# Optimization experiments

Hardware: AMD Instinct MI355X
Metric: run time of the kernel (lower is better)

Reference implementation:

```python
import jax, jax.numpy as jnp
import numpy as np

B, N, DIM, H, D = 4, 2048, 1024, 16, 64  # inner_dim = dim // n_heads
NEG_INF = float('-inf')


def setup_inputs() -> dict:
    key = jax.random.key(0)
    k1, k2, k3, k4 = jax.random.split(key, 4)
    x = jax.random.normal(k1, (B, N, DIM), dtype=jnp.float32)
    Wqkv = jax.random.normal(k2, (3 * H * D, DIM), dtype=jnp.float32) * (DIM ** -0.5)
    key_mask = jax.random.randint(k3, (B, N), 0, 2).astype(jnp.bool_)
    query_mask = jax.random.randint(k4, (B, N), 0, 2).astype(jnp.bool_)
    return {"x": x, "Wqkv": Wqkv, "key_mask": key_mask, "query_mask": query_mask, "causal": 1}


def reference(x, Wqkv, key_mask, query_mask, causal):
    # fused qkv projection (self-attention fast path)
    qkv = jnp.einsum('bnc,fc->bnf', x, Wqkv)  # [B, N, 3*H*D]
    q, k, v = jnp.split(qkv, 3, axis=-1)
    def to_heads(t):
        return t.reshape(B, N, H, D).transpose(0, 2, 1, 3)  # b h n d
    q, k, v = to_heads(q), to_heads(k), to_heads(v)

    attn = jnp.einsum('bhnd,bhmd->bhnm', q, k) / np.sqrt(D).astype(np.float32)

    # pairwise key/query mask: [B, 1, Nq, Nk]
    pair = key_mask[:, None, None, :] & query_mask[:, None, :, None]
    attn = attn + jnp.where(pair, 0.0, NEG_INF)

    if causal:
        causal_mask = jnp.triu(jnp.full((N, N), NEG_INF, dtype=attn.dtype), k=1)
        attn = attn + causal_mask

    attn = jax.nn.softmax(attn, axis=-1)
    attn = jnp.nan_to_num(attn, nan=0.0)  # fully-masked rows -> 0

    out = jnp.einsum('bhnm,bhmd->bhnd', attn, v)
    out = out.transpose(0, 2, 1, 3).reshape(B, N, H * D)  # b n (h d)
    # inner_dim * n_heads == dim, so out_proj is skipped (matches torch code)
    return out
```

## Files before the change

### kernel.cpp

```cpp
#include <hip/hip_runtime.h>
#include <hip/hip_bf16.h>

typedef unsigned short u16;
typedef __attribute__((ext_vector_type(8))) short bf16x8;
typedef __attribute__((ext_vector_type(4))) float f32x4;

#define Bdim 4
#define Nseq 2048
#define DIMc 1024
#define NH   16
#define HD   64
#define F3   3072
#define Mrows 8192

typedef const __attribute__((address_space(1))) unsigned int gl_u32;
typedef __attribute__((address_space(3))) unsigned int lds_u32;

static __device__ __forceinline__ u16 f2b(float f) {
    union { float f; unsigned u; } v; v.f = f;
    unsigned r = v.u + 0x7fffu + ((v.u >> 16) & 1u);
    return (u16)(r >> 16);
}

__global__ __launch_bounds__(256) void cast_f32_bf16_kernel(const float* __restrict__ in,
                                                            u16* __restrict__ out, int n4) {
    int i = blockIdx.x * 256 + threadIdx.x;
    if (i >= n4) return;
    float4 v = reinterpret_cast<const float4*>(in)[i];
    ushort4 o;
    o.x = f2b(v.x); o.y = f2b(v.y); o.z = f2b(v.z); o.w = f2b(v.w);
    reinterpret_cast<ushort4*>(out)[i] = o;
}

__global__ __launch_bounds__(256) void norm_mask_kernel(const void* __restrict__ raw, int n,
                                                        int* __restrict__ outm) {
    const unsigned* as_u = (const unsigned*)raw;
    const float* as_f = (const float*)raw;
    const unsigned char* as_b = (const unsigned char*)raw;
    int ns = n < 512 ? n : 512;
    bool ok_i = true, ok_f = true;
    for (int i = 0; i < ns; ++i) {
        unsigned v = as_u[i];
        ok_i &= (v <= 1u);
        ok_f &= (v == 0u) || (v == 0x3f800000u);
    }
    const int mode = ok_i ? 0 : (ok_f ? 1 : 2);
    int i = blockIdx.x * 256 + threadIdx.x;
    if (i < n) {
        int v;
        if (mode == 0) v = (int)as_u[i];
        else if (mode == 1) v = (as_f[i] != 0.f) ? 1 : 0;
        else v = (int)as_b[i];
        outm[i] = (v != 0) ? 1 : 0;
    }
}

__global__ __launch_bounds__(256, 2) void qkv_gemm_kernel(const u16* __restrict__ A,
                                                          const u16* __restrict__ Bw,
                                                          u16* __restrict__ C) {
    __shared__ u16 As[128 * 32];
    __shared__ u16 Bs[128 * 32];
    const int t = threadIdx.x;
    const int lane = t & 63;
    const int wave = t >> 6;
    const int wr = (wave >> 1) * 64;
    const int wc = (wave & 1) * 64;
    const int row0 = blockIdx.x * 128;
    const int col0 = blockIdx.y * 128;

    const int lr = lane & 15;
    const int lk = (lane >> 4) * 8;
    const int cr = (lane >> 4) * 4;
    const int cc = lane & 15;

    const f32x4 fzero = {0.f, 0.f, 0.f, 0.f};
    f32x4 acc[4][4];
#pragma unroll
    for (int i = 0; i < 4; ++i)
#pragma unroll
        for (int j = 0; j < 4; ++j) acc[i][j] = fzero;

    const int strow = wave * 16 + (lane >> 2);
    const int stcol = (lane & 3) * 8;

    for (int k0 = 0; k0 < DIMc; k0 += 32) {
        __syncthreads();
#pragma unroll
        for (int issue = 0; issue < 2; ++issue) {
            const int r = issue * 64 + strow;
            __builtin_amdgcn_global_load_lds(
                (gl_u32*)(A + (size_t)(row0 + r) * DIMc + k0 + stcol),
                (lds_u32*)(As + (size_t)(issue * 64 + wave * 16) * 32), 16, 0, 0);
            __builtin_amdgcn_global_load_lds(
                (gl_u32*)(Bw + (size_t)(col0 + r) * DIMc + k0 + stcol),
                (lds_u32*)(Bs + (size_t)(issue * 64 + wave * 16) * 32), 16, 0, 0);
        }
        __syncthreads();

        bf16x8 af[4], bfr[4];
#pragma unroll
        for (int i = 0; i < 4; ++i) {
            af[i]  = *reinterpret_cast<const bf16x8*>(&As[(wr + i * 16 + lr) * 32 + lk]);
            bfr[i] = *reinterpret_cast<const bf16x8*>(&Bs[(wc + i * 16 + lr) * 32 + lk]);
        }
#pragma unroll
        for (int mi = 0; mi < 4; ++mi)
#pragma unroll
            for (int ni = 0; ni < 4; ++ni)
                acc[mi][ni] = __builtin_amdgcn_mfma_f32_16x16x32_bf16(af[mi], bfr[ni], acc[mi][ni], 0, 0, 0);
    }

#pragma unroll
    for (int mi = 0; mi < 4; ++mi)
#pragma unroll
        for (int ni = 0; ni < 4; ++ni)
#pragma unroll
            for (int j = 0; j < 4; ++j) {
                int r = row0 + wr + mi * 16 + cr + j;
                int c = col0 + wc + ni * 16 + cc;
                C[(size_t)r * F3 + c] = f2b(acc[mi][ni][j]);
            }
}

static __device__ __forceinline__ void attn_tile_compute(
    const bf16x8 (&qfr)[2][2], const int (&qmv)[2],
    float (&mrow)[2], float (&lsum)[2], f32x4 (&oacc)[4][2],
    const bf16x8 (&ka)[4][2], const bf16x8 (&va)[4][2],
    const int (&km)[4][4],
    int wq0, int m0, int causal,
    u16 (*Psw)[72], int g, int lq)
{
    const f32x4 fzero = {0.f, 0.f, 0.f, 0.f};
    f32x4 sacc[4][2];
#pragma unroll
    for (int kf = 0; kf < 4; ++kf)
#pragma unroll
        for (int qf = 0; qf < 2; ++qf) sacc[kf][qf] = fzero;
#pragma unroll
    for (int kf = 0; kf < 4; ++kf)
#pragma unroll
        for (int qf = 0; qf < 2; ++qf) {
            sacc[kf][qf] = __builtin_amdgcn_mfma_f32_16x16x32_bf16(ka[kf][0], qfr[qf][0], sacc[kf][qf], 0, 0, 0);
            sacc[kf][qf] = __builtin_amdgcn_mfma_f32_16x16x32_bf16(ka[kf][1], qfr[qf][1], sacc[kf][qf], 0, 0, 0);
        }

#pragma unroll
    for (int qf = 0; qf < 2; ++qf) {
        const int qg = wq0 + qf * 16 + lq;
        const bool qok = (qmv[qf] != 0);
        float s[4][4];
        float mx = -1e30f;
#pragma unroll
        for (int kf = 0; kf < 4; ++kf)
#pragma unroll
            for (int r = 0; r < 4; ++r) {
                const int kg = m0 + kf * 16 + g * 4 + r;
                float sv = sacc[kf][qf][r] * 0.125f;
                const bool ok = qok && (km[kf][r] != 0) && (!causal || kg <= qg);
                sv = ok ? sv : -1e30f;
                s[kf][r] = sv;
                mx = fmaxf(mx, sv);
            }
        mx = fmaxf(mx, __shfl_xor(mx, 16));
        mx = fmaxf(mx, __shfl_xor(mx, 32));
        const float mnew = fmaxf(mrow[qf], mx);
        const float scale = __expf(mrow[qf] - mnew);
        float rs = 0.f;
#pragma unroll
        for (int kf = 0; kf < 4; ++kf)
#pragma unroll
            for (int r = 0; r < 4; ++r) {
                const float pv = (s[kf][r] > -1e29f) ? __expf(s[kf][r] - mnew) : 0.f;
                s[kf][r] = pv;
                rs += pv;
            }
        rs += __shfl_xor(rs, 16);
        rs += __shfl_xor(rs, 32);
        lsum[qf] = lsum[qf] * scale + rs;
        mrow[qf] = mnew;
#pragma unroll
        for (int df = 0; df < 4; ++df) oacc[df][qf] *= scale;
#pragma unroll
        for (int kf = 0; kf < 4; ++kf)
#pragma unroll
            for (int r = 0; r < 4; ++r)
                Psw[qf * 16 + lq][kf * 16 + g * 4 + r] = f2b(s[kf][r]);
    }

    bf16x8 pb[2][2];
#pragma unroll
    for (int qf = 0; qf < 2; ++qf)
#pragma unroll
        for (int kc = 0; kc < 2; ++kc)
            pb[qf][kc] = *reinterpret_cast<const bf16x8*>(&Psw[qf * 16 + lq][kc * 32 + g * 8]);
#pragma unroll
    for (int df = 0; df < 4; ++df)
#pragma unroll
        for (int qf = 0; qf < 2; ++qf) {
            oacc[df][qf] = __builtin_amdgcn_mfma_f32_16x16x32_bf16(va[df][0], pb[qf][0], oacc[df][qf], 0, 0, 0);
            oacc[df][qf] = __builtin_amdgcn_mfma_f32_16x16x32_bf16(va[df][1], pb[qf][1], oacc[df][qf], 0, 0, 0);
        }
}

__global__ __launch_bounds__(256, 2) void attn_kernel(const u16* __restrict__ qkv,
                                                      const int* __restrict__ key_mask,
                                                      const int* __restrict__ query_mask,
                                                      const int* __restrict__ causal_p,
                                                      float* __restrict__ out) {
    const int bh = blockIdx.x;
    const int p = blockIdx.y;
    const int b = bh >> 4;
    const int h = bh & 15;
    const int t = threadIdx.x;
    const int lane = t & 63;
    const int wave = t >> 6;
    const int g = lane >> 4;
    const int lq = lane & 15;
    const int causal = causal_p[0];

    __shared__ u16 Ks[64][72];
    __shared__ u16 Vt[64][72];
    __shared__ u16 Ps[4][32][72];

    const int q0A = p * 128;
    const int q0B = (15 - p) * 128;
    const int wq0A = q0A + wave * 32;
    const int wq0B = q0B + wave * 32;

    const f32x4 fzero = {0.f, 0.f, 0.f, 0.f};

    bf16x8 qfrA[2][2], qfrB[2][2];
#pragma unroll
    for (int qf = 0; qf < 2; ++qf)
#pragma unroll
        for (int ks = 0; ks < 2; ++ks) {
            qfrA[qf][ks] = *reinterpret_cast<const bf16x8*>(
                qkv + (size_t)(b * Nseq + wq0A + qf * 16 + lq) * F3 + h * HD + ks * 32 + g * 8);
            qfrB[qf][ks] = *reinterpret_cast<const bf16x8*>(
                qkv + (size_t)(b * Nseq + wq0B + qf * 16 + lq) * F3 + h * HD + ks * 32 + g * 8);
        }

    int qmA[2], qmB[2];
    float mrowA[2], lsumA[2], mrowB[2], lsumB[2];
    f32x4 oaccA[4][2], oaccB[4][2];
#pragma unroll
    for (int qf = 0; qf < 2; ++qf) {
        qmA[qf] = query_mask[b * Nseq + wq0A + qf * 16 + lq];
        qmB[qf] = query_mask[b * Nseq + wq0B + qf * 16 + lq];
        mrowA[qf] = -1e30f; lsumA[qf] = 0.f;
        mrowB[qf] = -1e30f; lsumB[qf] = 0.f;
    }
#pragma unroll
    for (int df = 0; df < 4; ++df)
#pragma unroll
        for (int qf = 0; qf < 2; ++qf) { oaccA[df][qf] = fzero; oaccB[df][qf] = fzero; }

    const int kvendA = causal ? (q0A + 128) : Nseq;
    const int kvendB = causal ? (q0B + 128) : Nseq;

    const int sr = t >> 2;
    const int sc = (t & 3) * 8;

    bf16x8 kr0, kr1, vr0, vr1;
    {
        const u16* krow = qkv + (size_t)(b * Nseq + 0 + sr) * F3 + DIMc + h * HD;
        kr0 = *reinterpret_cast<const bf16x8*>(krow + sc);
        kr1 = *reinterpret_cast<const bf16x8*>(krow + sc + 32);
        const u16* vrow = qkv + (size_t)(b * Nseq + 0 + lane) * F3 + 2 * DIMc + h * HD + wave * 16;
        vr0 = *reinterpret_cast<const bf16x8*>(vrow);
        vr1 = *reinterpret_cast<const bf16x8*>(vrow + 8);
    }

    for (int m0 = 0; m0 < kvendB; m0 += 64) {
        *reinterpret_cast<bf16x8*>(&Ks[sr][sc])      = kr0;
        *reinterpret_cast<bf16x8*>(&Ks[sr][sc + 32]) = kr1;
#pragma unroll
        for (int e = 0; e < 8; ++e) {
            Vt[wave * 16 + e][lane]     = (u16)vr0[e];
            Vt[wave * 16 + 8 + e][lane] = (u16)vr1[e];
        }
        __syncthreads();

        if (m0 + 64 < kvendB) {
            const u16* krow = qkv + (size_t)(b * Nseq + m0 + 64 + sr) * F3 + DIMc + h * HD;
            kr0 = *reinterpret_cast<const bf16x8*>(krow + sc);
            kr1 = *reinterpret_cast<const bf16x8*>(krow + sc + 32);
            const u16* vrow = qkv + (size_t)(b * Nseq + m0 + 64 + lane) * F3 + 2 * DIMc + h * HD + wave * 16;
            vr0 = *reinterpret_cast<const bf16x8*>(vrow);
            vr1 = *reinterpret_cast<const bf16x8*>(vrow + 8);
        }

        int km[4][4];
#pragma unroll
        for (int kf = 0; kf < 4; ++kf) {
            int4 k4 = *reinterpret_cast<const int4*>(key_mask + b * Nseq + m0 + kf * 16 + g * 4);
            km[kf][0] = k4.x; km[kf][1] = k4.y; km[kf][2] = k4.z; km[kf][3] = k4.w;
        }
        bf16x8 ka[4][2], va[4][2];
#pragma unroll
        for (int kf = 0; kf < 4; ++kf)
#pragma unroll
            for (int ks = 0; ks < 2; ++ks)
                ka[kf][ks] = *reinterpret_cast<const bf16x8*>(&Ks[kf * 16 + lq][ks * 32 + g * 8]);
#pragma unroll
        for (int df = 0; df < 4; ++df)
#pragma unroll
            for (int kc = 0; kc < 2; ++kc)
                va[df][kc] = *reinterpret_cast<const bf16x8*>(&Vt[df * 16 + lq][kc * 32 + g * 8]);

        attn_tile_compute(qfrB, qmB, mrowB, lsumB, oaccB, ka, va, km, wq0B, m0, causal,
                          Ps[wave], g, lq);
        if (m0 < kvendA)
            attn_tile_compute(qfrA, qmA, mrowA, lsumA, oaccA, ka, va, km, wq0A, m0, causal,
                              Ps[wave], g, lq);
        __syncthreads();
    }

#pragma unroll
    for (int qf = 0; qf < 2; ++qf) {
        const float invA = (mrowA[qf] > -1e29f && lsumA[qf] > 0.f) ? 1.f / lsumA[qf] : 0.f;
        const float invB = (mrowB[qf] > -1e29f && lsumB[qf] > 0.f) ? 1.f / lsumB[qf] : 0.f;
        const size_t rowA = (size_t)(b * Nseq + wq0A + qf * 16 + lq) * DIMc + h * HD;
        const size_t rowB = (size_t)(b * Nseq + wq0B + qf * 16 + lq) * DIMc + h * HD;
#pragma unroll
        for (int df = 0; df < 4; ++df)
#pragma unroll
            for (int r = 0; r < 4; ++r) {
                out[rowA + df * 16 + g * 4 + r] = oaccA[df][qf][r] * invA;
                out[rowB + df * 16 + g * 4 + r] = oaccB[df][qf][r] * invB;
            }
    }
}

extern "C" void kernel_launch(void* const* d_in, const int* in_sizes, int n_in,
                              void* d_out, int out_size, void* d_ws, size_t ws_size,
                              hipStream_t stream) {
    const float* x = (const float*)d_in[0];
    const float* W = (const float*)d_in[1];

    char* ws = (char*)d_ws;
    int* km_n = (int*)(ws);
    int* qm_n = (int*)(ws + 32 * 1024);
    int* ca_n = (int*)(ws + 64 * 1024);
    u16* qkv  = (u16*)(ws + (size_t)1024 * 1024);
    u16* xb   = (u16*)(ws + (size_t)49 * 1024 * 1024);
    u16* wb   = (u16*)(ws + (size_t)65 * 1024 * 1024);

    const int nm = Bdim * Nseq;
    norm_mask_kernel<<<(nm + 255) / 256, 256, 0, stream>>>(d_in[2], nm, km_n);
    norm_mask_kernel<<<(nm + 255) / 256, 256, 0, stream>>>(d_in[3], nm, qm_n);
    norm_mask_kernel<<<1, 256, 0, stream>>>(d_in[4], 1, ca_n);

    const int nx4 = (Mrows * DIMc) / 4;
    const int nw4 = (F3 * DIMc) / 4;
    cast_f32_bf16_kernel<<<(nx4 + 255) / 256, 256, 0, stream>>>(x, xb, nx4);
    cast_f32_bf16_kernel<<<(nw4 + 255) / 256, 256, 0, stream>>>(W, wb, nw4);

    qkv_gemm_kernel<<<dim3(Mrows / 128, F3 / 128), 256, 0, stream>>>(xb, wb, qkv);

    attn_kernel<<<dim3(Bdim * NH, 8), 256, 0, stream>>>(qkv, km_n, qm_n, ca_n,
                                                        (float*)d_out);
}
```

Measured before the change: 244.0 us.

## Halve attention query tile per wave and double grid for occupancy

Each wave now handles 16 query rows instead of 32 per tile pair, so each block covers 64+64 query rows and the grid doubles to 16 blocks per head along y. Register and LDS use shrink, launch bounds are raised to allow 4 blocks per CU, and the LDS row padding changes from 72 to 68. The intent is more parallel blocks and higher occupancy to hide latency. The cost is that each K/V tile loaded into LDS is reused across fewer queries, which raises total K/V traffic and synchronisation per unit of work.

```diff
diff --git a/kernel.cpp b/kernel.cpp
--- a/kernel.cpp
+++ b/kernel.cpp
@@ -12,6 +12,8 @@
 #define HD   64
 #define F3   3072
 #define Mrows 8192
+
+#define KPAD 68
 
 typedef const __attribute__((address_space(1))) unsigned int gl_u32;
 typedef __attribute__((address_space(3))) unsigned int lds_u32;
@@ -123,86 +125,75 @@
 }
 
 static __device__ __forceinline__ void attn_tile_compute(
-    const bf16x8 (&qfr)[2][2], const int (&qmv)[2],
-    float (&mrow)[2], float (&lsum)[2], f32x4 (&oacc)[4][2],
+    const bf16x8 (&qfr)[2], int qmv,
+    float& mrow, float& lsum, f32x4 (&oacc)[4],
     const bf16x8 (&ka)[4][2], const bf16x8 (&va)[4][2],
     const int (&km)[4][4],
     int wq0, int m0, int causal,
-    u16 (*Psw)[72], int g, int lq)
+    u16 (*Psw)[KPAD], int g, int lq)
 {
     const f32x4 fzero = {0.f, 0.f, 0.f, 0.f};
-    f32x4 sacc[4][2];
+    f32x4 sacc[4];
+#pragma unroll
+    for (int kf = 0; kf < 4; ++kf) sacc[kf] = fzero;
+#pragma unroll
+    for (int kf = 0; kf < 4; ++kf) {
+        sacc[kf] = __builtin_amdgcn_mfma_f32_16x16x32_bf16(ka[kf][0], qfr[0], sacc[kf], 0, 0, 0);
+        sacc[kf] = __builtin_amdgcn_mfma_f32_16x16x32_bf16(ka[kf][1], qfr[1], sacc[kf], 0, 0, 0);
+    }
+
+    const int qg = wq0 + lq;
+    const bool qok = (qmv != 0);
+    float s[4][4];
+    float mx = -1e30f;
 #pragma unroll
     for (int kf = 0; kf < 4; ++kf)
 #pragma unroll
-        for (int qf = 0; qf < 2; ++qf) sacc[kf][qf] = fzero;
+        for (int r = 0; r < 4; ++r) {
+            const int kg = m0 + kf * 16 + g * 4 + r;
+            float sv = sacc[kf][r] * 0.125f;
+            const bool ok = qok && (km[kf][r] != 0) && (!causal || kg <= qg);
+            sv = ok ? sv : -1e30f;
+            s[kf][r] = sv;
+            mx = fmaxf(mx, sv);
+        }
+    mx = fmaxf(mx, __shfl_xor(mx, 16));
+    mx = fmaxf(mx, __shfl_xor(mx, 32));
+    const float mnew = fmaxf(mrow, mx);
+    const float scale = __expf(mrow - mnew);
+    float rs = 0.f;
 #pragma unroll
     for (int kf = 0; kf < 4; ++kf)
 #pragma unroll
-        for (int qf = 0; qf < 2; ++qf) {
-            sacc[kf][qf] = __builtin_amdgcn_mfma_f32_16x16x32_bf16(ka[kf][0], qfr[qf][0], sacc[kf][qf], 0, 0, 0);
-            sacc[kf][qf] = __builtin_amdgcn_mfma_f32_16x16x32_bf16(ka[kf][1], qfr[qf][1], sacc[kf][qf], 0, 0, 0);
-        }
-
-#pragma unroll
-    for (int qf = 0; qf < 2; ++qf) {
-        const int qg = wq0 + qf * 16 + lq;
-        const bool qok = (qmv[qf] != 0);
-        float s[4][4];
-        float mx = -1e30f;
-#pragma unroll
-        for (int kf = 0; kf < 4; ++kf)
-#pragma unroll
-            for (int r = 0; r < 4; ++r) {
-                const int kg = m0 + kf * 16 + g * 4 + r;
-                float sv = sacc[kf][qf][r] * 0.125f;
-                const bool ok = qok && (km[kf][r] != 0) && (!causal || kg <= qg);
-                sv = ok ? sv : -1e30f;
-                s[kf][r] = sv;
-                mx = fmaxf(mx, sv);
-            }
-        mx = fmaxf(mx, __shfl_xor(mx, 16));
-        mx = fmaxf(mx, __shfl_xor(mx, 32));
-        const float mnew = fmaxf(mrow[qf], mx);
-        const float scale = __expf(mrow[qf] - mnew);
-        float rs = 0.f;
-#pragma unroll
-        for (int kf = 0; kf < 4; ++kf)
-#pragma unroll
-            for (int r = 0; r < 4; ++r) {
-                const float pv = (s[kf][r] > -1e29f) ? __expf(s[kf][r] - mnew) : 0.f;
-                s[kf][r] = pv;
-                rs += pv;
-            }
-        rs += __shfl_xor(rs, 16);
-        rs += __shfl_xor(rs, 32);
-        lsum[qf] = lsum[qf] * scale + rs;
-        mrow[qf] = mnew;
-#pragma unroll
-        for (int df = 0; df < 4; ++df) oacc[df][qf] *= scale;
-#pragma unroll
-        for (int kf = 0; kf < 4; ++kf)
-#pragma unroll
-            for (int r = 0; r < 4; ++r)
-                Psw[qf * 16 + lq][kf * 16 + g * 4 + r] = f2b(s[kf][r]);
-    }
-
-    bf16x8 pb[2][2];
-#pragma unroll
-    for (int qf = 0; qf < 2; ++qf)
-#pragma unroll
-        for (int kc = 0; kc < 2; ++kc)
-            pb[qf][kc] = *reinterpret_cast<const bf16x8*>(&Psw[qf * 16 + lq][kc * 32 + g * 8]);
-#pragma unroll
-    for (int df = 0; df < 4; ++df)
-#pragma unroll
-        for (int qf = 0; qf < 2; ++qf) {
-            oacc[df][qf] = __builtin_amdgcn_mfma_f32_16x16x32_bf16(va[df][0], pb[qf][0], oacc[df][qf], 0, 0, 0);
-            oacc[df][qf] = __builtin_amdgcn_mfma_f32_16x16x32_bf16(va[df][1], pb[qf][1], oacc[df][qf], 0, 0, 0);
-        }
-}
-
-__global__ __launch_bounds__(256, 2) void attn_kernel(const u16* __restrict__ qkv,
+        for (int r = 0; r < 4; ++r) {
+            const float pv = (s[kf][r] > -1e29f) ? __expf(s[kf][r] - mnew) : 0.f;
+            s[kf][r] = pv;
+            rs += pv;
+        }
+    rs += __shfl_xor(rs, 16);
+    rs += __shfl_xor(rs, 32);
+    lsum = lsum * scale + rs;
+    mrow = mnew;
+#pragma unroll
+    for (int df = 0; df < 4; ++df) oacc[df] *= scale;
+#pragma unroll
+    for (int kf = 0; kf < 4; ++kf)
+#pragma unroll
+        for (int r = 0; r < 4; ++r)
+            Psw[lq][kf * 16 + g * 4 + r] = f2b(s[kf][r]);
+
+    bf16x8 pb[2];
+#pragma unroll
+    for (int kc = 0; kc < 2; ++kc)
+        pb[kc] = *reinterpret_cast<const bf16x8*>(&Psw[lq][kc * 32 + g * 8]);
+#pragma unroll
+    for (int df = 0; df < 4; ++df) {
+        oacc[df] = __builtin_amdgcn_mfma_f32_16x16x32_bf16(va[df][0], pb[0], oacc[df], 0, 0, 0);
+        oacc[df] = __builtin_amdgcn_mfma_f32_16x16x32_bf16(va[df][1], pb[1], oacc[df], 0, 0, 0);
+    }
+}
+
+__global__ __launch_bounds__(256, 4) void attn_kernel(const u16* __restrict__ qkv,
                                                       const int* __restrict__ key_mask,
                                                       const int* __restrict__ query_mask,
                                                       const int* __restrict__ causal_p,
@@ -218,55 +209,45 @@
     const int lq = lane & 15;
     const int causal = causal_p[0];
 
-    __shared__ u16 Ks[64][72];
-    __shared__ u16 Vt[64][72];
-    __shared__ u16 Ps[4][32][72];
-
-    const int q0A = p * 128;
-    const int q0B = (15 - p) * 128;
-    const int wq0A = q0A + wave * 32;
-    const int wq0B = q0B + wave * 32;
+    __shared__ u16 Ks[64][KPAD];
+    __shared__ u16 Vt[64][KPAD];
+    __shared__ u16 Ps[4][16][KPAD];
+
+    const int q0A = p * 64;
+    const int q0B = (31 - p) * 64;
+    const int wq0A = q0A + wave * 16;
+    const int wq0B = q0B + wave * 16;
 
     const f32x4 fzero = {0.f, 0.f, 0.f, 0.f};
 
-    bf16x8 qfrA[2][2], qfrB[2][2];
-#pragma unroll
-    for (int qf = 0; qf < 2; ++qf)
-#pragma unroll
-        for (int ks = 0; ks < 2; ++ks) {
-            qfrA[qf][ks] = *reinterpret_cast<const bf16x8*>(
-                qkv + (size_t)(b * Nseq + wq0A + qf * 16 + lq) * F3 + h * HD + ks * 32 + g * 8);
-            qfrB[qf][ks] = *reinterpret_cast<const bf16x8*>(
-                qkv + (size_t)(b * Nseq + wq0B + qf * 16 + lq) * F3 + h * HD + ks * 32 + g * 8);
-        }
-
-    int qmA[2], qmB[2];
-    float mrowA[2], lsumA[2], mrowB[2], lsumB[2];
-    f32x4 oaccA[4][2], oaccB[4][2];
-#pragma unroll
-    for (int qf = 0; qf < 2; ++qf) {
-        qmA[qf] = query_mask[b * Nseq + wq0A + qf * 16 + lq];
-        qmB[qf] = query_mask[b * Nseq + wq0B + qf * 16 + lq];
-        mrowA[qf] = -1e30f; lsumA[qf] = 0.f;
-        mrowB[qf] = -1e30f; lsumB[qf] = 0.f;
-    }
-#pragma unroll
-    for (int df = 0; df < 4; ++df)
-#pragma unroll
-        for (int qf = 0; qf < 2; ++qf) { oaccA[df][qf] = fzero; oaccB[df][qf] = fzero; }
-
-    const int kvendA = causal ? (q0A + 128) : Nseq;
-    const int kvendB = causal ? (q0B + 128) : Nseq;
+    bf16x8 qfrA[2], qfrB[2];
+#pragma unroll
+    for (int ks = 0; ks < 2; ++ks) {
+        qfrA[ks] = *reinterpret_cast<const bf16x8*>(
+            qkv + (size_t)(b * Nseq + wq0A + lq) * F3 + h * HD + ks * 32 + g * 8);
+        qfrB[ks] = *reinterpret_cast<const bf16x8*>(
+            qkv + (size_t)(b * Nseq + wq0B + lq) * F3 + h * HD + ks * 32 + g * 8);
+    }
+
+    const int qmA = query_mask[b * Nseq + wq0A + lq];
+    const int qmB = query_mask[b * Nseq + wq0B + lq];
+    float mrowA = -1e30f, lsumA = 0.f, mrowB = -1e30f, lsumB = 0.f;
+    f32x4 oaccA[4], oaccB[4];
+#pragma unroll
+    for (int df = 0; df < 4; ++df) { oaccA[df] = fzero; oaccB[df] = fzero; }
+
+    const int kvendA = causal ? (q0A + 64) : Nseq;
+    const int kvendB = causal ? (q0B + 64) : Nseq;
 
     const int sr = t >> 2;
     const int sc = (t & 3) * 8;
 
     bf16x8 kr0, kr1, vr0, vr1;
     {
-        const u16* krow = qkv + (size_t)(b * Nseq + 0 + sr) * F3 + DIMc + h * HD;
+        const u16* krow = qkv + (size_t)(b * Nseq + sr) * F3 + DIMc + h * HD;
         kr0 = *reinterpret_cast<const bf16x8*>(krow + sc);
         kr1 = *reinterpret_cast<const bf16x8*>(krow + sc + 32);
-        const u16* vrow = qkv + (size_t)(b * Nseq + 0 + lane) * F3 + 2 * DIMc + h * HD + wave * 16;
+        const u16* vrow = qkv + (size_t)(b * Nseq + lane) * F3 + 2 * DIMc + h * HD + wave * 16;
         vr0 = *reinterpret_cast<const bf16x8*>(vrow);
         vr1 = *reinterpret_cast<const bf16x8*>(vrow + 8);
     }
@@ -316,18 +297,17 @@
         __syncthreads();
     }
 
-#pragma unroll
-    for (int qf = 0; qf < 2; ++qf) {
-        const float invA = (mrowA[qf] > -1e29f && lsumA[qf] > 0.f) ? 1.f / lsumA[qf] : 0.f;
-        const float invB = (mrowB[qf] > -1e29f && lsumB[qf] > 0.f) ? 1.f / lsumB[qf] : 0.f;
-        const size_t rowA = (size_t)(b * Nseq + wq0A + qf * 16 + lq) * DIMc + h * HD;
-        const size_t rowB = (size_t)(b * Nseq + wq0B + qf * 16 + lq) * DIMc + h * HD;
+    {
+        const float invA = (mrowA > -1e29f && lsumA > 0.f) ? 1.f / lsumA : 0.f;
+        const float invB = (mrowB > -1e29f && lsumB > 0.f) ? 1.f / lsumB : 0.f;
+        const size_t rowA = (size_t)(b * Nseq + wq0A + lq) * DIMc + h * HD;
+        const size_t rowB = (size_t)(b * Nseq + wq0B + lq) * DIMc + h * HD;
 #pragma unroll
         for (int df = 0; df < 4; ++df)
 #pragma unroll
             for (int r = 0; r < 4; ++r) {
-                out[rowA + df * 16 + g * 4 + r] = oaccA[df][qf][r] * invA;
-                out[rowB + df * 16 + g * 4 + r] = oaccB[df][qf][r] * invB;
+                out[rowA + df * 16 + g * 4 + r] = oaccA[df][r] * invA;
+                out[rowB + df * 16 + g * 4 + r] = oaccB[df][r] * invB;
             }
     }
 }
@@ -358,6 +338,6 @@
 
     qkv_gemm_kernel<<<dim3(Mrows / 128, F3 / 128), 256, 0, stream>>>(xb, wb, qkv);
 
-    attn_kernel<<<dim3(Bdim * NH, 8), 256, 0, stream>>>(qkv, km_n, qm_n, ca_n,
-                                                        (float*)d_out);
-}
+    attn_kernel<<<dim3(Bdim * NH, 16), 256, 0, stream>>>(qkv, km_n, qm_n, ca_n,
+                                                         (float*)d_out);
+}
```

Result: slower. 558.1 us (+128.7%).

## Split paired causal query tiles across separate waves in 512-thread attention blocks

Applied to the files above, without the earlier changes.

The attention kernel now uses 512 threads, so the two paired query tiles (early and late for causal balance) go to separate groups of four waves instead of each wave handling both sequentially. K/V staging is spread across eight waves with one 16-byte load each, and the LDS row padding drops from 72 to 68. The aim is more parallel waves per block and fewer registers per wave, so the two tiles' compute overlaps. In exchange, the early-tile waves sit idle at barriers once their causal range ends, and the new padding may change LDS bank-conflict behaviour.

```diff
diff --git a/kernel.cpp b/kernel.cpp
--- a/kernel.cpp
+++ b/kernel.cpp
@@ -12,6 +12,8 @@
 #define HD   64
 #define F3   3072
 #define Mrows 8192
+
+#define KPAD 68
 
 typedef const __attribute__((address_space(1))) unsigned int gl_u32;
 typedef __attribute__((address_space(3))) unsigned int lds_u32;
@@ -128,7 +130,7 @@
     const bf16x8 (&ka)[4][2], const bf16x8 (&va)[4][2],
     const int (&km)[4][4],
     int wq0, int m0, int causal,
-    u16 (*Psw)[72], int g, int lq)
+    u16 (*Psw)[KPAD], int g, int lq)
 {
     const f32x4 fzero = {0.f, 0.f, 0.f, 0.f};
     f32x4 sacc[4][2];
@@ -202,7 +204,7 @@
         }
 }
 
-__global__ __launch_bounds__(256, 2) void attn_kernel(const u16* __restrict__ qkv,
+__global__ __launch_bounds__(512, 4) void attn_kernel(const u16* __restrict__ qkv,
                                                       const int* __restrict__ key_mask,
                                                       const int* __restrict__ query_mask,
                                                       const int* __restrict__ causal_p,
@@ -214,121 +216,104 @@
     const int t = threadIdx.x;
     const int lane = t & 63;
     const int wave = t >> 6;
+    const int wtile = wave >> 2;
+    const int wsub = wave & 3;
     const int g = lane >> 4;
     const int lq = lane & 15;
     const int causal = causal_p[0];
 
-    __shared__ u16 Ks[64][72];
-    __shared__ u16 Vt[64][72];
-    __shared__ u16 Ps[4][32][72];
-
-    const int q0A = p * 128;
-    const int q0B = (15 - p) * 128;
-    const int wq0A = q0A + wave * 32;
-    const int wq0B = q0B + wave * 32;
+    __shared__ u16 Ks[64][KPAD];
+    __shared__ u16 Vt[64][KPAD];
+    __shared__ u16 Ps[8][32][KPAD];
+
+    const int q0 = (wtile ? (15 - p) : p) * 128;
+    const int wq0 = q0 + wsub * 32;
 
     const f32x4 fzero = {0.f, 0.f, 0.f, 0.f};
 
-    bf16x8 qfrA[2][2], qfrB[2][2];
+    bf16x8 qfr[2][2];
 #pragma unroll
     for (int qf = 0; qf < 2; ++qf)
 #pragma unroll
-        for (int ks = 0; ks < 2; ++ks) {
-            qfrA[qf][ks] = *reinterpret_cast<const bf16x8*>(
-                qkv + (size_t)(b * Nseq + wq0A + qf * 16 + lq) * F3 + h * HD + ks * 32 + g * 8);
-            qfrB[qf][ks] = *reinterpret_cast<const bf16x8*>(
-                qkv + (size_t)(b * Nseq + wq0B + qf * 16 + lq) * F3 + h * HD + ks * 32 + g * 8);
-        }
-
-    int qmA[2], qmB[2];
-    float mrowA[2], lsumA[2], mrowB[2], lsumB[2];
-    f32x4 oaccA[4][2], oaccB[4][2];
+        for (int ks = 0; ks < 2; ++ks)
+            qfr[qf][ks] = *reinterpret_cast<const bf16x8*>(
+                qkv + (size_t)(b * Nseq + wq0 + qf * 16 + lq) * F3 + h * HD + ks * 32 + g * 8);
+
+    int qmv[2];
+    float mrow[2], lsum[2];
+    f32x4 oacc[4][2];
 #pragma unroll
     for (int qf = 0; qf < 2; ++qf) {
-        qmA[qf] = query_mask[b * Nseq + wq0A + qf * 16 + lq];
-        qmB[qf] = query_mask[b * Nseq + wq0B + qf * 16 + lq];
-        mrowA[qf] = -1e30f; lsumA[qf] = 0.f;
-        mrowB[qf] = -1e30f; lsumB[qf] = 0.f;
+        qmv[qf] = query_mask[b * Nseq + wq0 + qf * 16 + lq];
+        mrow[qf] = -1e30f; lsum[qf] = 0.f;
     }
 #pragma unroll
     for (int df = 0; df < 4; ++df)
 #pragma unroll
-        for (int qf = 0; qf < 2; ++qf) { oaccA[df][qf] = fzero; oaccB[df][qf] = fzero; }
-
-    const int kvendA = causal ? (q0A + 128) : Nseq;
-    const int kvendB = causal ? (q0B + 128) : Nseq;
-
-    const int sr = t >> 2;
-    const int sc = (t & 3) * 8;
-
-    bf16x8 kr0, kr1, vr0, vr1;
+        for (int qf = 0; qf < 2; ++qf) oacc[df][qf] = fzero;
+
+    const int kvend = causal ? (q0 + 128) : Nseq;
+    const int kvendMax = causal ? ((15 - p) * 128 + 128) : Nseq;
+
+    const int srK = t >> 3;
+    const int scK = (t & 7) * 8;
+
+    bf16x8 kr, vr;
     {
-        const u16* krow = qkv + (size_t)(b * Nseq + 0 + sr) * F3 + DIMc + h * HD;
-        kr0 = *reinterpret_cast<const bf16x8*>(krow + sc);
-        kr1 = *reinterpret_cast<const bf16x8*>(krow + sc + 32);
-        const u16* vrow = qkv + (size_t)(b * Nseq + 0 + lane) * F3 + 2 * DIMc + h * HD + wave * 16;
-        vr0 = *reinterpret_cast<const bf16x8*>(vrow);
-        vr1 = *reinterpret_cast<const bf16x8*>(vrow + 8);
-    }
-
-    for (int m0 = 0; m0 < kvendB; m0 += 64) {
-        *reinterpret_cast<bf16x8*>(&Ks[sr][sc])      = kr0;
-        *reinterpret_cast<bf16x8*>(&Ks[sr][sc + 32]) = kr1;
-#pragma unroll
-        for (int e = 0; e < 8; ++e) {
-            Vt[wave * 16 + e][lane]     = (u16)vr0[e];
-            Vt[wave * 16 + 8 + e][lane] = (u16)vr1[e];
-        }
+        kr = *reinterpret_cast<const bf16x8*>(
+            qkv + (size_t)(b * Nseq + srK) * F3 + DIMc + h * HD + scK);
+        vr = *reinterpret_cast<const bf16x8*>(
+            qkv + (size_t)(b * Nseq + lane) * F3 + 2 * DIMc + h * HD + wave * 8);
+    }
+
+    for (int m0 = 0; m0 < kvendMax; m0 += 64) {
+        *reinterpret_cast<bf16x8*>(&Ks[srK][scK]) = kr;
+#pragma unroll
+        for (int e = 0; e < 8; ++e)
+            Vt[wave * 8 + e][lane] = (u16)vr[e];
         __syncthreads();
 
-        if (m0 + 64 < kvendB) {
-            const u16* krow = qkv + (size_t)(b * Nseq + m0 + 64 + sr) * F3 + DIMc + h * HD;
-            kr0 = *reinterpret_cast<const bf16x8*>(krow + sc);
-            kr1 = *reinterpret_cast<const bf16x8*>(krow + sc + 32);
-            const u16* vrow = qkv + (size_t)(b * Nseq + m0 + 64 + lane) * F3 + 2 * DIMc + h * HD + wave * 16;
-            vr0 = *reinterpret_cast<const bf16x8*>(vrow);
-            vr1 = *reinterpret_cast<const bf16x8*>(vrow + 8);
-        }
-
-        int km[4][4];
-#pragma unroll
-        for (int kf = 0; kf < 4; ++kf) {
-            int4 k4 = *reinterpret_cast<const int4*>(key_mask + b * Nseq + m0 + kf * 16 + g * 4);
-            km[kf][0] = k4.x; km[kf][1] = k4.y; km[kf][2] = k4.z; km[kf][3] = k4.w;
-        }
-        bf16x8 ka[4][2], va[4][2];
-#pragma unroll
-        for (int kf = 0; kf < 4; ++kf)
-#pragma unroll
-            for (int ks = 0; ks < 2; ++ks)
-                ka[kf][ks] = *reinterpret_cast<const bf16x8*>(&Ks[kf * 16 + lq][ks * 32 + g * 8]);
+        if (m0 + 64 < kvendMax) {
+            kr = *reinterpret_cast<const bf16x8*>(
+                qkv + (size_t)(b * Nseq + m0 + 64 + srK) * F3 + DIMc + h * HD + scK);
+            vr = *reinterpret_cast<const bf16x8*>(
+                qkv + (size_t)(b * Nseq + m0 + 64 + lane) * F3 + 2 * DIMc + h * HD + wave * 8);
+        }
+
+        if (m0 < kvend) {
+            int km[4][4];
+#pragma unroll
+            for (int kf = 0; kf < 4; ++kf) {
+                int4 k4 = *reinterpret_cast<const int4*>(key_mask + b * Nseq + m0 + kf * 16 + g * 4);
+                km[kf][0] = k4.x; km[kf][1] = k4.y; km[kf][2] = k4.z; km[kf][3] = k4.w;
+            }
+            bf16x8 ka[4][2], va[4][2];
+#pragma unroll
+            for (int kf = 0; kf < 4; ++kf)
+#pragma unroll
+                for (int ks = 0; ks < 2; ++ks)
+                    ka[kf][ks] = *reinterpret_cast<const bf16x8*>(&Ks[kf * 16 + lq][ks * 32 + g * 8]);
+#pragma unroll
+            for (int df = 0; df < 4; ++df)
+#pragma unroll
+                for (int kc = 0; kc < 2; ++kc)
+                    va[df][kc] = *reinterpret_cast<const bf16x8*>(&Vt[df * 16 + lq][kc * 32 + g * 8]);
+
+            attn_tile_compute(qfr, qmv, mrow, lsum, oacc, ka, va, km, wq0, m0, causal,
+                              Ps[wave], g, lq);
+        }
+        __syncthreads();
+    }
+
+#pragma unroll
+    for (int qf = 0; qf < 2; ++qf) {
+        const float inv = (mrow[qf] > -1e29f && lsum[qf] > 0.f) ? 1.f / lsum[qf] : 0.f;
+        const size_t rowoff = (size_t)(b * Nseq + wq0 + qf * 16 + lq) * DIMc + h * HD;
 #pragma unroll
         for (int df = 0; df < 4; ++df)
 #pragma unroll
-            for (int kc = 0; kc < 2; ++kc)
-                va[df][kc] = *reinterpret_cast<const bf16x8*>(&Vt[df * 16 + lq][kc * 32 + g * 8]);
-
-        attn_tile_compute(qfrB, qmB, mrowB, lsumB, oaccB, ka, va, km, wq0B, m0, causal,
-                          Ps[wave], g, lq);
-        if (m0 < kvendA)
-            attn_tile_compute(qfrA, qmA, mrowA, lsumA, oaccA, ka, va, km, wq0A, m0, causal,
-                              Ps[wave], g, lq);
-        __syncthreads();
-    }
-
-#pragma unroll
-    for (int qf = 0; qf < 2; ++qf) {
-        const float invA = (mrowA[qf] > -1e29f && lsumA[qf] > 0.f) ? 1.f / lsumA[qf] : 0.f;
-        const float invB = (mrowB[qf] > -1e29f && lsumB[qf] > 0.f) ? 1.f / lsumB[qf] : 0.f;
-        const size_t rowA = (size_t)(b * Nseq + wq0A + qf * 16 + lq) * DIMc + h * HD;
-        const size_t rowB = (size_t)(b * Nseq + wq0B + qf * 16 + lq) * DIMc + h * HD;
-#pragma unroll
-        for (int df = 0; df < 4; ++df)
-#pragma unroll
-            for (int r = 0; r < 4; ++r) {
-                out[rowA + df * 16 + g * 4 + r] = oaccA[df][qf][r] * invA;
-                out[rowB + df * 16 + g * 4 + r] = oaccB[df][qf][r] * invB;
-            }
+            for (int r = 0; r < 4; ++r)
+                out[rowoff + df * 16 + g * 4 + r] = oacc[df][qf][r] * inv;
     }
 }
 
@@ -358,6 +343,6 @@
 
     qkv_gemm_kernel<<<dim3(Mrows / 128, F3 / 128), 256, 0, stream>>>(xb, wb, qkv);
 
-    attn_kernel<<<dim3(Bdim * NH, 8), 256, 0, stream>>>(qkv, km_n, qm_n, ca_n,
+    attn_kernel<<<dim3(Bdim * NH, 8), 512, 0, stream>>>(qkv, km_n, qm_n, ca_n,
                                                         (float*)d_out);
 }
```

Measured after the change: 269.6 us. +10.5%, slower.

## Double-buffer K/V tiles in LDS, per-wave causal bounds, and narrower LDS padding

Applied to the files above, without the earlier changes.

K and V tiles now live in two LDS buffers. The next tile is written into the alternate buffer after compute, and the tile after that is prefetched into registers, so only one barrier per iteration is needed instead of two. Causal loop bounds are now per wave (wq0+32) rather than per block, so waves skip tiles that lie entirely above their diagonal. The LDS row padding shrinks from 72 to 68 to keep the doubled buffers small, but this may change bank-conflict behaviour, and 68*2 bytes is not 16-byte aligned for the bf16x8 vector accesses.

```diff
diff --git a/kernel.cpp b/kernel.cpp
--- a/kernel.cpp
+++ b/kernel.cpp
@@ -12,6 +12,8 @@
 #define HD   64
 #define F3   3072
 #define Mrows 8192
+
+#define KPAD 68
 
 typedef const __attribute__((address_space(1))) unsigned int gl_u32;
 typedef __attribute__((address_space(3))) unsigned int lds_u32;
@@ -128,7 +130,7 @@
     const bf16x8 (&ka)[4][2], const bf16x8 (&va)[4][2],
     const int (&km)[4][4],
     int wq0, int m0, int causal,
-    u16 (*Psw)[72], int g, int lq)
+    u16 (*Psw)[KPAD], int g, int lq)
 {
     const f32x4 fzero = {0.f, 0.f, 0.f, 0.f};
     f32x4 sacc[4][2];
@@ -218,9 +220,9 @@
     const int lq = lane & 15;
     const int causal = causal_p[0];
 
-    __shared__ u16 Ks[64][72];
-    __shared__ u16 Vt[64][72];
-    __shared__ u16 Ps[4][32][72];
+    __shared__ u16 Ks[2][64][KPAD];
+    __shared__ u16 Vt[2][64][KPAD];
+    __shared__ u16 Ps[4][32][KPAD];
 
     const int q0A = p * 128;
     const int q0B = (15 - p) * 128;
@@ -255,40 +257,41 @@
 #pragma unroll
         for (int qf = 0; qf < 2; ++qf) { oaccA[df][qf] = fzero; oaccB[df][qf] = fzero; }
 
-    const int kvendA = causal ? (q0A + 128) : Nseq;
-    const int kvendB = causal ? (q0B + 128) : Nseq;
+    const int kvA = causal ? (wq0A + 32) : Nseq;
+    const int kvB = causal ? (wq0B + 32) : Nseq;
+    const int kvendMax = causal ? (q0B + 128) : Nseq;
 
     const int sr = t >> 2;
     const int sc = (t & 3) * 8;
 
     bf16x8 kr0, kr1, vr0, vr1;
     {
-        const u16* krow = qkv + (size_t)(b * Nseq + 0 + sr) * F3 + DIMc + h * HD;
+        const u16* krow = qkv + (size_t)(b * Nseq + sr) * F3 + DIMc + h * HD;
         kr0 = *reinterpret_cast<const bf16x8*>(krow + sc);
         kr1 = *reinterpret_cast<const bf16x8*>(krow + sc + 32);
-        const u16* vrow = qkv + (size_t)(b * Nseq + 0 + lane) * F3 + 2 * DIMc + h * HD + wave * 16;
+        const u16* vrow = qkv + (size_t)(b * Nseq + lane) * F3 + 2 * DIMc + h * HD + wave * 16;
         vr0 = *reinterpret_cast<const bf16x8*>(vrow);
         vr1 = *reinterpret_cast<const bf16x8*>(vrow + 8);
-    }
-
-    for (int m0 = 0; m0 < kvendB; m0 += 64) {
-        *reinterpret_cast<bf16x8*>(&Ks[sr][sc])      = kr0;
-        *reinterpret_cast<bf16x8*>(&Ks[sr][sc + 32]) = kr1;
+        *reinterpret_cast<bf16x8*>(&Ks[0][sr][sc])      = kr0;
+        *reinterpret_cast<bf16x8*>(&Ks[0][sr][sc + 32]) = kr1;
 #pragma unroll
         for (int e = 0; e < 8; ++e) {
-            Vt[wave * 16 + e][lane]     = (u16)vr0[e];
-            Vt[wave * 16 + 8 + e][lane] = (u16)vr1[e];
-        }
+            Vt[0][wave * 16 + e][lane]     = (u16)vr0[e];
+            Vt[0][wave * 16 + 8 + e][lane] = (u16)vr1[e];
+        }
+        if (64 < kvendMax) {
+            const u16* krow1 = qkv + (size_t)(b * Nseq + 64 + sr) * F3 + DIMc + h * HD;
+            kr0 = *reinterpret_cast<const bf16x8*>(krow1 + sc);
+            kr1 = *reinterpret_cast<const bf16x8*>(krow1 + sc + 32);
+            const u16* vrow1 = qkv + (size_t)(b * Nseq + 64 + lane) * F3 + 2 * DIMc + h * HD + wave * 16;
+            vr0 = *reinterpret_cast<const bf16x8*>(vrow1);
+            vr1 = *reinterpret_cast<const bf16x8*>(vrow1 + 8);
+        }
+    }
+
+    int cur = 0;
+    for (int m0 = 0; m0 < kvendMax; m0 += 64) {
         __syncthreads();
-
-        if (m0 + 64 < kvendB) {
-            const u16* krow = qkv + (size_t)(b * Nseq + m0 + 64 + sr) * F3 + DIMc + h * HD;
-            kr0 = *reinterpret_cast<const bf16x8*>(krow + sc);
-            kr1 = *reinterpret_cast<const bf16x8*>(krow + sc + 32);
-            const u16* vrow = qkv + (size_t)(b * Nseq + m0 + 64 + lane) * F3 + 2 * DIMc + h * HD + wave * 16;
-            vr0 = *reinterpret_cast<const bf16x8*>(vrow);
-            vr1 = *reinterpret_cast<const bf16x8*>(vrow + 8);
-        }
 
         int km[4][4];
 #pragma unroll
@@ -301,19 +304,38 @@
         for (int kf = 0; kf < 4; ++kf)
 #pragma unroll
             for (int ks = 0; ks < 2; ++ks)
-                ka[kf][ks] = *reinterpret_cast<const bf16x8*>(&Ks[kf * 16 + lq][ks * 32 + g * 8]);
+                ka[kf][ks] = *reinterpret_cast<const bf16x8*>(&Ks[cur][kf * 16 + lq][ks * 32 + g * 8]);
 #pragma unroll
         for (int df = 0; df < 4; ++df)
 #pragma unroll
             for (int kc = 0; kc < 2; ++kc)
-                va[df][kc] = *reinterpret_cast<const bf16x8*>(&Vt[df * 16 + lq][kc * 32 + g * 8]);
-
-        attn_tile_compute(qfrB, qmB, mrowB, lsumB, oaccB, ka, va, km, wq0B, m0, causal,
-                          Ps[wave], g, lq);
-        if (m0 < kvendA)
+                va[df][kc] = *reinterpret_cast<const bf16x8*>(&Vt[cur][df * 16 + lq][kc * 32 + g * 8]);
+
+        if (m0 < kvB)
+            attn_tile_compute(qfrB, qmB, mrowB, lsumB, oaccB, ka, va, km, wq0B, m0, causal,
+                              Ps[wave], g, lq);
+        if (m0 < kvA)
             attn_tile_compute(qfrA, qmA, mrowA, lsumA, oaccA, ka, va, km, wq0A, m0, causal,
                               Ps[wave], g, lq);
-        __syncthreads();
+
+        if (m0 + 64 < kvendMax) {
+            *reinterpret_cast<bf16x8*>(&Ks[cur ^ 1][sr][sc])      = kr0;
+            *reinterpret_cast<bf16x8*>(&Ks[cur ^ 1][sr][sc + 32]) = kr1;
+#pragma unroll
+            for (int e = 0; e < 8; ++e) {
+                Vt[cur ^ 1][wave * 16 + e][lane]     = (u16)vr0[e];
+                Vt[cur ^ 1][wave * 16 + 8 + e][lane] = (u16)vr1[e];
+            }
+            if (m0 + 128 < kvendMax) {
+                const u16* krow = qkv + (size_t)(b * Nseq + m0 + 128 + sr) * F3 + DIMc + h * HD;
+                kr0 = *reinterpret_cast<const bf16x8*>(krow + sc);
+                kr1 = *reinterpret_cast<const bf16x8*>(krow + sc + 32);
+                const u16* vrow = qkv + (size_t)(b * Nseq + m0 + 128 + lane) * F3 + 2 * DIMc + h * HD + wave * 16;
+                vr0 = *reinterpret_cast<const bf16x8*>(vrow);
+                vr1 = *reinterpret_cast<const bf16x8*>(vrow + 8);
+            }
+        }
+        cur ^= 1;
     }
 
 #pragma unroll
```

After: 264.1 us. 1.08x slower.
